# Kernel optimization log

Measured on AMD Instinct MI355X. Metric: run time of the kernel, lower is better.

## Reference

```python
import jax, jax.numpy as jnp
import numpy as np

NUM_HEADS = 16
NUM_HIDDENS = 1024
NEG_INF = -1e6


def setup_inputs() -> dict:
    key = jax.random.key(0)
    ks = jax.random.split(key, 8)
    B, S, D = 2, 2048, NUM_HIDDENS
    scale = 1.0 / np.sqrt(D)
    return {
        "q": jax.random.normal(ks[0], (B, S, D), jnp.float32),
        "k": jax.random.normal(ks[1], (B, S, D), jnp.float32),
        "v": jax.random.normal(ks[2], (B, S, D), jnp.float32),
        # nn.Linear weights have shape (out_features, in_features)
        "Wq": jax.random.normal(ks[3], (D, D), jnp.float32) * scale,
        "Wk": jax.random.normal(ks[4], (D, D), jnp.float32) * scale,
        "Wv": jax.random.normal(ks[5], (D, D), jnp.float32) * scale,
        "Wo": jax.random.normal(ks[6], (D, D), jnp.float32) * scale,
        "valid_len": jax.random.randint(ks[7], (B,), 1, 2048 + 1, jnp.int32),
    }


def _unpack_heads(x, nh):
    # (B, S, H) -> (B*nh, S, H//nh), matching Unpack_base_head
    B, S, H = x.shape
    return x.reshape(B, S, nh, H // nh).transpose(0, 2, 1, 3).reshape(B * nh, S, H // nh)


def _merge_heads(x, nh):
    # Faithful to Merge_base_head: (B*nh, S, dh) -> (B, nh, S, dh)
    # -> permute(0,2,3,1) -> (B, S, dh, nh) -> (B, S, dh*nh)
    Bnh, S, dh = x.shape
    B = Bnh // nh
    x = x.reshape(B, nh, S, dh).transpose(0, 2, 3, 1)
    return x.reshape(B, S, dh * nh)


def reference(q, k, v, Wq, Wk, Wv, Wo, valid_len):
    nh = NUM_HEADS
    # projections (bias=False); Linear: x @ W.T
    qh = _unpack_heads(q @ Wq.T, nh)  # (B*nh, S, dh)
    kh = _unpack_heads(k @ Wk.T, nh)
    vh = _unpack_heads(v @ Wv.T, nh)
    dh = qh.shape[-1]
    scores = jnp.einsum("bqd,bkd->bqk", qh, kh) / jnp.sqrt(jnp.float32(dh))
    # repeat_interleave valid_len by num_heads along dim 0
    vl = jnp.repeat(valid_len, nh)  # (B*nh,)
    key_pos = jnp.arange(scores.shape[-1])  # (S,)
    mask = key_pos[None, None, :] < vl[:, None, None]  # (B*nh, 1, S)
    scores = jnp.where(mask, scores, NEG_INF)
    attn = jax.nn.softmax(scores, axis=-1)  # dropout=0.0 (eval) -> identity
    out = jnp.einsum("bqk,bkd->bqd", attn, vh)  # (B*nh, S, dh)
    out = _merge_heads(out, nh) @ Wo.T  # (B, S, H)
    return out, attn
```

## Files before the change

### kernel.cpp

```cpp
#include <hip/hip_runtime.h>
#include <stdint.h>

#define SB 2048
#define DB 1024
#define NHB 16
#define DHB 64

typedef __attribute__((ext_vector_type(8))) short short8;
typedef __attribute__((ext_vector_type(4))) short short4v;
typedef __attribute__((ext_vector_type(4))) float f32x4;

__device__ __forceinline__ unsigned short f2bf(float f) {
  union { float f; uint32_t u; } v; v.f = f;
  uint32_t u = v.u;
  return (unsigned short)((u + 0x7FFFu + ((u >> 16) & 1u)) >> 16);
}

__device__ __forceinline__ void gld16(const void* g, void* l) {
  __builtin_amdgcn_global_load_lds(
      (const __attribute__((address_space(1))) void*)g,
      (__attribute__((address_space(3))) void*)l, 16, 0, 0);
}

__device__ __forceinline__ int xcd_swz(int bid, int nwg) {
  return (bid & 7) * (nwg >> 3) + (bid >> 3);
}

struct ConvArgs {
  const float* s[7];
  unsigned short* d[7];
  int n[7];
};

__global__ __launch_bounds__(256) void conv_kernel(ConvArgs a) {
  const int t = blockIdx.y;
  const float* __restrict__ src = a.s[t];
  unsigned short* __restrict__ dst = a.d[t];
  const int n8 = a.n[t] >> 3;
  for (int i = blockIdx.x * 256 + threadIdx.x; i < n8; i += gridDim.x * 256) {
    const f32x4* p = (const f32x4*)src + (size_t)i * 2;
    f32x4 x = p[0], y = p[1];
    short8 o;
    o[0] = (short)f2bf(x[0]); o[1] = (short)f2bf(x[1]);
    o[2] = (short)f2bf(x[2]); o[3] = (short)f2bf(x[3]);
    o[4] = (short)f2bf(y[0]); o[5] = (short)f2bf(y[1]);
    o[6] = (short)f2bf(y[2]); o[7] = (short)f2bf(y[3]);
    *(short8*)(dst + (size_t)i * 8) = o;
  }
}

struct GemmArgs {
  const unsigned short* A[3];
  const unsigned short* B[3];
  void* O[3];
  int mode[3];
};

__global__ __launch_bounds__(256) void gemm128(GemmArgs ga) {
  __shared__ unsigned short SH[17408];
  unsigned short* Ab = SH;
  unsigned short* Bb = SH + 8192;

  const int z = blockIdx.y;
  const unsigned short* __restrict__ A = ga.A[z];
  const unsigned short* __restrict__ Bw = ga.B[z];
  const int mode = ga.mode[z];

  const int tid = threadIdx.x;
  const int w = tid >> 6, lane = tid & 63;
  const int g = lane >> 4, li = lane & 15;
  const int wm = w >> 1, wn = w & 1;
  const int l = xcd_swz(blockIdx.x, 256);
  const int m0 = (l >> 3) * 128, n0 = (l & 7) * 128;

  const int srow = lane >> 3;
  const int sg = (lane & 7) ^ srow;

  f32x4 acc[4][4];
  #pragma unroll
  for (int i = 0; i < 4; ++i)
    #pragma unroll
    for (int j = 0; j < 4; ++j)
      #pragma unroll
      for (int e = 0; e < 4; ++e) acc[i][j][e] = 0.f;

  for (int k0 = 0; k0 < DB; k0 += 64) {
    __syncthreads();
    #pragma unroll
    for (int i = 0; i < 4; ++i) {
      int c = w * 4 + i;
      gld16(A + (size_t)(m0 + c * 8 + srow) * DB + k0 + sg * 8, Ab + c * 512);
      gld16(Bw + (size_t)(n0 + c * 8 + srow) * DB + k0 + sg * 8, Bb + c * 512);
    }
    __syncthreads();
    short8 af[4][2], bf[4][2];
    #pragma unroll
    for (int mf = 0; mf < 4; ++mf)
      #pragma unroll
      for (int ks = 0; ks < 2; ++ks)
        af[mf][ks] = *(const short8*)&Ab[(wm * 64 + mf * 16 + li) * 64 +
                                         (((ks * 4 + g) ^ (li & 7)) << 3)];
    #pragma unroll
    for (int nf = 0; nf < 4; ++nf)
      #pragma unroll
      for (int ks = 0; ks < 2; ++ks)
        bf[nf][ks] = *(const short8*)&Bb[(wn * 64 + nf * 16 + li) * 64 +
                                         (((ks * 4 + g) ^ (li & 7)) << 3)];
    #pragma unroll
    for (int ks = 0; ks < 2; ++ks)
      #pragma unroll
      for (int mf = 0; mf < 4; ++mf)
        #pragma unroll
        for (int nf = 0; nf < 4; ++nf)
          acc[mf][nf] = __builtin_amdgcn_mfma_f32_16x16x32_bf16(
              af[mf][ks], bf[nf][ks], acc[mf][nf], 0, 0, 0);
  }

  if (mode == 0) {
    unsigned short* O = (unsigned short*)ga.O[z];
    #pragma unroll
    for (int mf = 0; mf < 4; ++mf)
      #pragma unroll
      for (int nf = 0; nf < 4; ++nf)
        #pragma unroll
        for (int r = 0; r < 4; ++r) {
          int row = m0 + wm * 64 + mf * 16 + g * 4 + r;
          int col = n0 + wn * 64 + nf * 16 + li;
          int b_ = row >> 11, s_ = row & 2047;
          int h = col >> 6, dp = col & 63;
          O[((size_t)(b_ * NHB + h) * SB + s_) * DHB + dp] = f2bf(acc[mf][nf][r]);
        }
  } else if (mode == 1) {
    unsigned short* O = (unsigned short*)ga.O[z];
    __syncthreads();
    #pragma unroll
    for (int mf = 0; mf < 4; ++mf)
      #pragma unroll
      for (int nf = 0; nf < 4; ++nf) {
        short4v pk;
        #pragma unroll
        for (int r = 0; r < 4; ++r) pk[r] = (short)f2bf(acc[mf][nf][r]);
        *(short4v*)&SH[(size_t)(wn * 64 + nf * 16 + li) * 136 +
                       wm * 64 + mf * 16 + g * 4] = pk;
      }
    __syncthreads();
    int c = tid >> 1, rh = tid & 1;
    int col = n0 + c;
    int h = col >> 6, dp = col & 63;
    int b_ = m0 >> 11, s0 = (m0 & 2047) + rh * 64;
    unsigned short* dst = O + ((size_t)(b_ * NHB + h) * DHB + dp) * SB + s0;
    #pragma unroll
    for (int j = 0; j < 8; ++j)
      *(short8*)(dst + j * 8) = *(const short8*)&SH[c * 136 + rh * 64 + j * 8];
  } else {
    float* O = (float*)ga.O[z];
    #pragma unroll
    for (int mf = 0; mf < 4; ++mf)
      #pragma unroll
      for (int nf = 0; nf < 4; ++nf)
        #pragma unroll
        for (int r = 0; r < 4; ++r) {
          int row = m0 + wm * 64 + mf * 16 + g * 4 + r;
          int col = n0 + wn * 64 + nf * 16 + li;
          O[(size_t)row * DB + col] = acc[mf][nf][r];
        }
  }
}

__global__ __launch_bounds__(256) void attn_kernel(
    const unsigned short* __restrict__ Qh, const unsigned short* __restrict__ Kh,
    const unsigned short* __restrict__ Vt, const int* __restrict__ valid_len,
    float* __restrict__ attn_out, unsigned short* __restrict__ Mg)
{
  __shared__ unsigned short Kb[2][4096];
  __shared__ unsigned short Vb[2][4096];
  __shared__ unsigned short QP[128][72];

  const int tid = threadIdx.x;
  const int wave = tid >> 6, lane = tid & 63;
  const int g = lane >> 4, li = lane & 15;
  const int lsw = xcd_swz(blockIdx.x, 512);
  const int q0 = (lsw & 15) * 128;
  const int bh = lsw >> 4;
  const int b_ = bh >> 4;
  const int vl = valid_len[b_];
  const int nkt = min(32, (vl + 63) >> 6);

  const int srow = lane >> 3;
  const int sg = (lane & 7) ^ srow;

  {
    int qr = tid >> 1, half = (tid & 1) * 32;
    const unsigned short* src = Qh + ((size_t)bh * SB + q0 + qr) * DHB + half;
    #pragma unroll
    for (int j = 0; j < 4; ++j)
      *(short8*)&QP[qr][half + j * 8] = *(const short8*)(src + j * 8);
  }
  __syncthreads();

  short8 qa[2][2];
  #pragma unroll
  for (int qf = 0; qf < 2; ++qf)
    #pragma unroll
    for (int ks = 0; ks < 2; ++ks)
      qa[qf][ks] = *(const short8*)&QP[wave * 32 + qf * 16 + li][ks * 32 + g * 8];

  float mQ[2] = {-1e30f, -1e30f}, lQ[2] = {0.f, 0.f};

  {
    #pragma unroll
    for (int i = 0; i < 2; ++i) {
      int c = wave * 2 + i;
      gld16(Kh + ((size_t)bh * SB + 0 + c * 8 + srow) * DHB + sg * 8,
            &Kb[0][c * 512]);
    }
    int cur = 0;
    for (int kti = 0; kti < nkt; ++kti) {
      const int kt = kti * 64;
      __syncthreads();
      if (kti + 1 < nkt) {
        #pragma unroll
        for (int i = 0; i < 2; ++i) {
          int c = wave * 2 + i;
          gld16(Kh + ((size_t)bh * SB + kt + 64 + c * 8 + srow) * DHB + sg * 8,
                &Kb[cur ^ 1][c * 512]);
        }
      }
      f32x4 sc[2][4];
      #pragma unroll
      for (int qf = 0; qf < 2; ++qf)
        #pragma unroll
        for (int nf = 0; nf < 4; ++nf)
          #pragma unroll
          for (int j = 0; j < 4; ++j) sc[qf][nf][j] = 0.f;
      #pragma unroll
      for (int ks = 0; ks < 2; ++ks)
        #pragma unroll
        for (int nf = 0; nf < 4; ++nf) {
          short8 kbf = *(const short8*)&Kb[cur][(nf * 16 + li) * 64 +
                                               (((ks * 4 + g) ^ (li & 7)) << 3)];
          #pragma unroll
          for (int qf = 0; qf < 2; ++qf)
            sc[qf][nf] = __builtin_amdgcn_mfma_f32_16x16x32_bf16(
                kbf, qa[qf][ks], sc[qf][nf], 0, 0, 0);
        }
      #pragma unroll
      for (int qf = 0; qf < 2; ++qf) {
        float tm = -1e30f;
        #pragma unroll
        for (int nf = 0; nf < 4; ++nf)
          #pragma unroll
          for (int r = 0; r < 4; ++r) {
            int key = kt + nf * 16 + g * 4 + r;
            float s = sc[qf][nf][r] * 0.125f;
            s = (key < vl) ? s : -1e6f;
            sc[qf][nf][r] = s;
            tm = fmaxf(tm, s);
          }
        float mo = mQ[qf], mn = fmaxf(mo, tm);
        float la = lQ[qf] * __expf(mo - mn);
        #pragma unroll
        for (int nf = 0; nf < 4; ++nf)
          #pragma unroll
          for (int r = 0; r < 4; ++r) la += __expf(sc[qf][nf][r] - mn);
        mQ[qf] = mn;
        lQ[qf] = la;
      }
      cur ^= 1;
    }
  }
  __syncthreads();

  float rlQ[2];
  #pragma unroll
  for (int qf = 0; qf < 2; ++qf) {
    float M = mQ[qf];
    M = fmaxf(M, __shfl_xor(M, 16));
    M = fmaxf(M, __shfl_xor(M, 32));
    float L = lQ[qf] * __expf(mQ[qf] - M);
    L += __shfl_xor(L, 16);
    L += __shfl_xor(L, 32);
    mQ[qf] = M;
    rlQ[qf] = 1.f / L;
  }

  f32x4 oacc[2][4];
  #pragma unroll
  for (int qf = 0; qf < 2; ++qf)
    #pragma unroll
    for (int nf = 0; nf < 4; ++nf)
      #pragma unroll
      for (int j = 0; j < 4; ++j) oacc[qf][nf][j] = 0.f;

  {
    #pragma unroll
    for (int i = 0; i < 2; ++i) {
      int c = wave * 2 + i;
      gld16(Kh + ((size_t)bh * SB + c * 8 + srow) * DHB + sg * 8, &Kb[0][c * 512]);
      gld16(Vt + ((size_t)bh * DHB + c * 8 + srow) * SB + 0 + sg * 8, &Vb[0][c * 512]);
    }
    int cur = 0;
    for (int kti = 0; kti < nkt; ++kti) {
      const int kt = kti * 64;
      __syncthreads();
      if (kti + 1 < nkt) {
        #pragma unroll
        for (int i = 0; i < 2; ++i) {
          int c = wave * 2 + i;
          gld16(Kh + ((size_t)bh * SB + kt + 64 + c * 8 + srow) * DHB + sg * 8,
                &Kb[cur ^ 1][c * 512]);
          gld16(Vt + ((size_t)bh * DHB + c * 8 + srow) * SB + kt + 64 + sg * 8,
                &Vb[cur ^ 1][c * 512]);
        }
      }
      f32x4 sc[2][4];
      #pragma unroll
      for (int qf = 0; qf < 2; ++qf)
        #pragma unroll
        for (int nf = 0; nf < 4; ++nf)
          #pragma unroll
          for (int j = 0; j < 4; ++j) sc[qf][nf][j] = 0.f;
      #pragma unroll
      for (int ks = 0; ks < 2; ++ks)
        #pragma unroll
        for (int nf = 0; nf < 4; ++nf) {
          short8 kbf = *(const short8*)&Kb[cur][(nf * 16 + li) * 64 +
                                               (((ks * 4 + g) ^ (li & 7)) << 3)];
          #pragma unroll
          for (int qf = 0; qf < 2; ++qf)
            sc[qf][nf] = __builtin_amdgcn_mfma_f32_16x16x32_bf16(
                kbf, qa[qf][ks], sc[qf][nf], 0, 0, 0);
        }
      #pragma unroll
      for (int qf = 0; qf < 2; ++qf) {
        int qrow = q0 + wave * 32 + qf * 16 + li;
        #pragma unroll
        for (int nf = 0; nf < 4; ++nf) {
          short4v pk;
          #pragma unroll
          for (int r = 0; r < 4; ++r) {
            int key = kt + nf * 16 + g * 4 + r;
            float s = sc[qf][nf][r] * 0.125f;
            s = (key < vl) ? s : -1e6f;
            float p = __expf(s - mQ[qf]) * rlQ[qf];
            sc[qf][nf][r] = p;
            pk[r] = (short)f2bf(p);
          }
          __builtin_nontemporal_store(
              sc[qf][nf],
              (f32x4*)(attn_out + (size_t)bh * SB * SB + (size_t)qrow * SB +
                       kt + nf * 16 + g * 4));
          *(short4v*)&QP[wave * 32 + qf * 16 + li][nf * 16 + g * 4] = pk;
        }
      }
      asm volatile("s_waitcnt lgkmcnt(0)" ::: "memory");
      __builtin_amdgcn_sched_barrier(0);
      #pragma unroll
      for (int ks = 0; ks < 2; ++ks) {
        short8 vbf[4];
        #pragma unroll
        for (int nf = 0; nf < 4; ++nf)
          vbf[nf] = *(const short8*)&Vb[cur][(nf * 16 + li) * 64 +
                                             (((ks * 4 + g) ^ (li & 7)) << 3)];
        #pragma unroll
        for (int qf = 0; qf < 2; ++qf) {
          short8 pa = *(const short8*)&QP[wave * 32 + qf * 16 + li][ks * 32 + g * 8];
          #pragma unroll
          for (int nf = 0; nf < 4; ++nf)
            oacc[qf][nf] = __builtin_amdgcn_mfma_f32_16x16x32_bf16(
                pa, vbf[nf], oacc[qf][nf], 0, 0, 0);
        }
      }
      cur ^= 1;
    }
  }

  {
    int c0 = nkt * 64;
    int rem4 = (SB - c0) >> 2;
    if (rem4 > 0) {
      f32x4 z;
      z[0] = 0.f; z[1] = 0.f; z[2] = 0.f; z[3] = 0.f;
      for (int row = 0; row < 128; ++row) {
        float* dst = attn_out + (size_t)bh * SB * SB + (size_t)(q0 + row) * SB + c0;
        for (int c = tid; c < rem4; c += 256)
          __builtin_nontemporal_store(z, (f32x4*)dst + c);
      }
    }
  }

  const int h = bh & 15;
  #pragma unroll
  for (int qf = 0; qf < 2; ++qf)
    #pragma unroll
    for (int nf = 0; nf < 4; ++nf)
      #pragma unroll
      for (int r = 0; r < 4; ++r) {
        int qrow = q0 + wave * 32 + qf * 16 + g * 4 + r;
        int dp = nf * 16 + li;
        Mg[((size_t)b_ * SB + qrow) * DB + dp * NHB + h] = f2bf(oacc[qf][nf][r]);
      }
}

extern "C" void kernel_launch(void* const* d_in, const int* in_sizes, int n_in,
                              void* d_out, int out_size, void* d_ws, size_t ws_size,
                              hipStream_t stream) {
  const float* q  = (const float*)d_in[0];
  const float* k  = (const float*)d_in[1];
  const float* v  = (const float*)d_in[2];
  const float* Wq = (const float*)d_in[3];
  const float* Wk = (const float*)d_in[4];
  const float* Wv = (const float*)d_in[5];
  const float* Wo = (const float*)d_in[6];
  const int* vlen = (const int*)d_in[7];

  const size_t HS = (size_t)2 * NHB * SB * DHB;
  const size_t WS = (size_t)DB * DB;

  unsigned short* ws = (unsigned short*)d_ws;
  unsigned short* qb  = ws;
  unsigned short* kb  = qb + HS;
  unsigned short* vb  = kb + HS;
  unsigned short* Wqb = vb + HS;
  unsigned short* Wkb = Wqb + WS;
  unsigned short* Wvb = Wkb + WS;
  unsigned short* Wob = Wvb + WS;
  unsigned short* Qh  = Wob + WS;
  unsigned short* Kh  = Qh + HS;
  unsigned short* Vt  = Kh + HS;
  unsigned short* Mg  = qb;

  float* out  = (float*)d_out;
  float* attn = out + (size_t)2 * SB * DB;

  ConvArgs ca;
  ca.s[0] = q;  ca.d[0] = qb;  ca.n[0] = (int)HS;
  ca.s[1] = k;  ca.d[1] = kb;  ca.n[1] = (int)HS;
  ca.s[2] = v;  ca.d[2] = vb;  ca.n[2] = (int)HS;
  ca.s[3] = Wq; ca.d[3] = Wqb; ca.n[3] = (int)WS;
  ca.s[4] = Wk; ca.d[4] = Wkb; ca.n[4] = (int)WS;
  ca.s[5] = Wv; ca.d[5] = Wvb; ca.n[5] = (int)WS;
  ca.s[6] = Wo; ca.d[6] = Wob; ca.n[6] = (int)WS;

  GemmArgs pa;
  pa.A[0] = qb;  pa.A[1] = kb;  pa.A[2] = vb;
  pa.B[0] = Wqb; pa.B[1] = Wkb; pa.B[2] = Wvb;
  pa.O[0] = Qh;  pa.O[1] = Kh;  pa.O[2] = Vt;
  pa.mode[0] = 0; pa.mode[1] = 0; pa.mode[2] = 1;

  GemmArgs oa;
  oa.A[0] = Mg; oa.B[0] = Wob; oa.O[0] = out; oa.mode[0] = 2;
  oa.A[1] = Mg; oa.B[1] = Wob; oa.O[1] = out; oa.mode[1] = 2;
  oa.A[2] = Mg; oa.B[2] = Wob; oa.O[2] = out; oa.mode[2] = 2;

  dim3 blk(256);
  conv_kernel<<<dim3(1024, 7), blk, 0, stream>>>(ca);
  gemm128<<<dim3(256, 3), blk, 0, stream>>>(pa);
  attn_kernel<<<dim3(512), blk, 0, stream>>>(Qh, Kh, Vt, vlen, attn, Mg);
  gemm128<<<dim3(256, 1), blk, 0, stream>>>(oa);
}
```

Before: 256.8 us.

## Add MFMA priority hints, pad QP, and use dedicated 128x64 output projection kernel

Wraps the MFMA blocks in the projection GEMM and the attention kernel with s_setprio so waves issuing matrix ops get scheduling priority. It also pads the QP shared buffer rows to change the LDS bank mapping and drops an explicit lgkmcnt wait plus sched barrier before the PV matmul. The output projection moves from the 256-block 128x128 GEMM to a new 512-block kernel with 128x64 tiles, giving more blocks for better CU fill, and the old fp32 output mode is removed. Removing the explicit wait relies on the compiler inserting the needed LDS waits for the QP writes before they are read.

```diff
diff --git a/kernel.cpp b/kernel.cpp
--- a/kernel.cpp
+++ b/kernel.cpp
@@ -106,6 +106,7 @@
       for (int ks = 0; ks < 2; ++ks)
         bf[nf][ks] = *(const short8*)&Bb[(wn * 64 + nf * 16 + li) * 64 +
                                          (((ks * 4 + g) ^ (li & 7)) << 3)];
+    __builtin_amdgcn_s_setprio(1);
     #pragma unroll
     for (int ks = 0; ks < 2; ++ks)
       #pragma unroll
@@ -114,6 +115,7 @@
         for (int nf = 0; nf < 4; ++nf)
           acc[mf][nf] = __builtin_amdgcn_mfma_f32_16x16x32_bf16(
               af[mf][ks], bf[nf][ks], acc[mf][nf], 0, 0, 0);
+    __builtin_amdgcn_s_setprio(0);
   }
 
   if (mode == 0) {
@@ -130,7 +132,7 @@
           int h = col >> 6, dp = col & 63;
           O[((size_t)(b_ * NHB + h) * SB + s_) * DHB + dp] = f2bf(acc[mf][nf][r]);
         }
-  } else if (mode == 1) {
+  } else {
     unsigned short* O = (unsigned short*)ga.O[z];
     __syncthreads();
     #pragma unroll
@@ -152,18 +154,6 @@
     #pragma unroll
     for (int j = 0; j < 8; ++j)
       *(short8*)(dst + j * 8) = *(const short8*)&SH[c * 136 + rh * 64 + j * 8];
-  } else {
-    float* O = (float*)ga.O[z];
-    #pragma unroll
-    for (int mf = 0; mf < 4; ++mf)
-      #pragma unroll
-      for (int nf = 0; nf < 4; ++nf)
-        #pragma unroll
-        for (int r = 0; r < 4; ++r) {
-          int row = m0 + wm * 64 + mf * 16 + g * 4 + r;
-          int col = n0 + wn * 64 + nf * 16 + li;
-          O[(size_t)row * DB + col] = acc[mf][nf][r];
-        }
   }
 }
 
@@ -174,7 +164,7 @@
 {
   __shared__ unsigned short Kb[2][4096];
   __shared__ unsigned short Vb[2][4096];
-  __shared__ unsigned short QP[128][72];
+  __shared__ unsigned short QP[128][88];
 
   const int tid = threadIdx.x;
   const int wave = tid >> 6, lane = tid & 63;
@@ -233,6 +223,7 @@
         for (int nf = 0; nf < 4; ++nf)
           #pragma unroll
           for (int j = 0; j < 4; ++j) sc[qf][nf][j] = 0.f;
+      __builtin_amdgcn_s_setprio(1);
       #pragma unroll
       for (int ks = 0; ks < 2; ++ks)
         #pragma unroll
@@ -244,6 +235,7 @@
             sc[qf][nf] = __builtin_amdgcn_mfma_f32_16x16x32_bf16(
                 kbf, qa[qf][ks], sc[qf][nf], 0, 0, 0);
         }
+      __builtin_amdgcn_s_setprio(0);
       #pragma unroll
       for (int qf = 0; qf < 2; ++qf) {
         float tm = -1e30f;
@@ -320,6 +312,7 @@
         for (int nf = 0; nf < 4; ++nf)
           #pragma unroll
           for (int j = 0; j < 4; ++j) sc[qf][nf][j] = 0.f;
+      __builtin_amdgcn_s_setprio(1);
       #pragma unroll
       for (int ks = 0; ks < 2; ++ks)
         #pragma unroll
@@ -331,6 +324,7 @@
             sc[qf][nf] = __builtin_amdgcn_mfma_f32_16x16x32_bf16(
                 kbf, qa[qf][ks], sc[qf][nf], 0, 0, 0);
         }
+      __builtin_amdgcn_s_setprio(0);
       #pragma unroll
       for (int qf = 0; qf < 2; ++qf) {
         int qrow = q0 + wave * 32 + qf * 16 + li;
@@ -353,8 +347,7 @@
           *(short4v*)&QP[wave * 32 + qf * 16 + li][nf * 16 + g * 4] = pk;
         }
       }
-      asm volatile("s_waitcnt lgkmcnt(0)" ::: "memory");
-      __builtin_amdgcn_sched_barrier(0);
+      __builtin_amdgcn_s_setprio(1);
       #pragma unroll
       for (int ks = 0; ks < 2; ++ks) {
         short8 vbf[4];
@@ -371,6 +364,7 @@
                 pa, vbf[nf], oacc[qf][nf], 0, 0, 0);
         }
       }
+      __builtin_amdgcn_s_setprio(0);
       cur ^= 1;
     }
   }
@@ -399,6 +393,96 @@
         int qrow = q0 + wave * 32 + qf * 16 + g * 4 + r;
         int dp = nf * 16 + li;
         Mg[((size_t)b_ * SB + qrow) * DB + dp * NHB + h] = f2bf(oacc[qf][nf][r]);
+      }
+}
+
+__global__ __launch_bounds__(256) void outproj_kernel(
+    const unsigned short* __restrict__ A, const unsigned short* __restrict__ Bw,
+    float* __restrict__ Out)
+{
+  __shared__ unsigned short SH[12288];
+  unsigned short* Ab = SH;
+  unsigned short* Bb = SH + 8192;
+
+  const int tid = threadIdx.x;
+  const int w = tid >> 6, lane = tid & 63;
+  const int g = lane >> 4, li = lane & 15;
+  const int wm = w >> 1, wn = w & 1;
+  const int l = xcd_swz(blockIdx.x, 512);
+  const int m0 = (l >> 4) * 128, n0 = (l & 15) * 64;
+
+  const int srow = lane >> 3;
+  const int sg = (lane & 7) ^ srow;
+
+  int a_off[4][2], b_off[2][2];
+  #pragma unroll
+  for (int mf = 0; mf < 4; ++mf) {
+    int row = wm * 64 + mf * 16 + li;
+    #pragma unroll
+    for (int ks = 0; ks < 2; ++ks)
+      a_off[mf][ks] = row * 64 + (((ks * 4 + g) ^ (li & 7)) << 3);
+  }
+  #pragma unroll
+  for (int nf = 0; nf < 2; ++nf) {
+    int row = wn * 32 + nf * 16 + li;
+    #pragma unroll
+    for (int ks = 0; ks < 2; ++ks)
+      b_off[nf][ks] = row * 64 + (((ks * 4 + g) ^ (li & 7)) << 3);
+  }
+
+  f32x4 acc[4][2];
+  #pragma unroll
+  for (int i = 0; i < 4; ++i)
+    #pragma unroll
+    for (int j = 0; j < 2; ++j)
+      #pragma unroll
+      for (int e = 0; e < 4; ++e) acc[i][j][e] = 0.f;
+
+  for (int k0 = 0; k0 < DB; k0 += 64) {
+    __syncthreads();
+    #pragma unroll
+    for (int i = 0; i < 4; ++i) {
+      int c = w * 4 + i;
+      gld16(A + (size_t)(m0 + c * 8 + srow) * DB + k0 + sg * 8, Ab + c * 512);
+    }
+    #pragma unroll
+    for (int i = 0; i < 2; ++i) {
+      int c = w * 2 + i;
+      gld16(Bw + (size_t)(n0 + c * 8 + srow) * DB + k0 + sg * 8, Bb + c * 512);
+    }
+    __syncthreads();
+    short8 af[4][2], bf[2][2];
+    #pragma unroll
+    for (int mf = 0; mf < 4; ++mf)
+      #pragma unroll
+      for (int ks = 0; ks < 2; ++ks)
+        af[mf][ks] = *(const short8*)&Ab[a_off[mf][ks]];
+    #pragma unroll
+    for (int nf = 0; nf < 2; ++nf)
+      #pragma unroll
+      for (int ks = 0; ks < 2; ++ks)
+        bf[nf][ks] = *(const short8*)&Bb[b_off[nf][ks]];
+    __builtin_amdgcn_s_setprio(1);
+    #pragma unroll
+    for (int ks = 0; ks < 2; ++ks)
+      #pragma unroll
+      for (int mf = 0; mf < 4; ++mf)
+        #pragma unroll
+        for (int nf = 0; nf < 2; ++nf)
+          acc[mf][nf] = __builtin_amdgcn_mfma_f32_16x16x32_bf16(
+              af[mf][ks], bf[nf][ks], acc[mf][nf], 0, 0, 0);
+    __builtin_amdgcn_s_setprio(0);
+  }
+
+  #pragma unroll
+  for (int mf = 0; mf < 4; ++mf)
+    #pragma unroll
+    for (int nf = 0; nf < 2; ++nf)
+      #pragma unroll
+      for (int r = 0; r < 4; ++r) {
+        int row = m0 + wm * 64 + mf * 16 + g * 4 + r;
+        int col = n0 + wn * 32 + nf * 16 + li;
+        Out[(size_t)row * DB + col] = acc[mf][nf][r];
       }
 }
 
@@ -448,14 +532,9 @@
   pa.O[0] = Qh;  pa.O[1] = Kh;  pa.O[2] = Vt;
   pa.mode[0] = 0; pa.mode[1] = 0; pa.mode[2] = 1;
 
-  GemmArgs oa;
-  oa.A[0] = Mg; oa.B[0] = Wob; oa.O[0] = out; oa.mode[0] = 2;
-  oa.A[1] = Mg; oa.B[1] = Wob; oa.O[1] = out; oa.mode[1] = 2;
-  oa.A[2] = Mg; oa.B[2] = Wob; oa.O[2] = out; oa.mode[2] = 2;
-
   dim3 blk(256);
   conv_kernel<<<dim3(1024, 7), blk, 0, stream>>>(ca);
   gemm128<<<dim3(256, 3), blk, 0, stream>>>(pa);
   attn_kernel<<<dim3(512), blk, 0, stream>>>(Qh, Kh, Vt, vlen, attn, Mg);
-  gemm128<<<dim3(256, 1), blk, 0, stream>>>(oa);
-}
+  outproj_kernel<<<dim3(512), blk, 0, stream>>>(Mg, Wob, out);
+}
```

After: 247.2 us. 3.7% less time.
